# Optimization experiments

Measured on AMD Instinct MI355X. Metric: run time of the kernel, lower is better.

The kernel has to match this reference:

```python
import jax, jax.numpy as jnp
import numpy as np

BITS = 4
OFF = 8          # 2**(BITS-1)
QLEVELS = 15.0   # 2**BITS - 1
IN_F, OUT_F, FP_F, TOKENS = 4096, 4096, 256, 4096
INT_F = IN_F - FP_F


def unpack_i4(w_packed):
    """Invert pack_to_i4: packed uint8 col k holds signed int4 cols (2k: low nibble, 2k+1: high)."""
    lo = (w_packed & 0x0F).astype(jnp.int8)
    hi = ((w_packed >> 4) & 0x0F).astype(jnp.int8)
    lo = jnp.where(lo >= 8, lo - 16, lo)
    hi = jnp.where(hi >= 8, hi - 16, hi)
    return jnp.stack([lo, hi], axis=-1).reshape(w_packed.shape[0], -1)  # (out, int_features)


def setup_inputs() -> dict:
    key = jax.random.key(0)
    k1, k2, k3, k4, k5 = jax.random.split(key, 5)
    x = jax.random.normal(k1, (1, TOKENS, IN_F), dtype=jnp.float16)
    perm = jax.random.permutation(k2, IN_F)
    fp_indices = jnp.sort(perm[:FP_F]).astype(jnp.int64)
    int_indices = jnp.sort(perm[FP_F:]).astype(jnp.int64)
    # signed int4 weight values in [-8, 7], packed two-per-byte like pack_to_i4
    w_vals = jax.random.randint(k3, (OUT_F, INT_F), -8, 8, dtype=jnp.int8)
    u = (w_vals.astype(jnp.int32) & 0x0F).astype(jnp.uint8)
    int_weight = (u[:, 0::2] | (u[:, 1::2] << 4)).astype(jnp.uint8)  # (out, INT_F//2)
    weights_scales = (jax.random.uniform(k4, (OUT_F, 1)) * 0.01 + 1e-3).astype(jnp.float16)
    # reduced_w = row-sum of the dequantized int-column weights (as in from_float)
    reduced_w = (w_vals.astype(jnp.float32).sum(axis=1, keepdims=True)
                 * weights_scales.astype(jnp.float32)).T.astype(jnp.float16)  # (1, out)
    fp_weight = (jax.random.normal(k5, (OUT_F, FP_F)) * 0.02).astype(jnp.float16)
    bias = jnp.zeros((OUT_F,), dtype=jnp.float16)
    return {"x": x, "int_weight": int_weight, "weights_scales": weights_scales,
            "reduced_w": reduced_w, "fp_weight": fp_weight, "bias": bias,
            "int_indices": int_indices, "fp_indices": fp_indices}


def reference(x, int_weight, weights_scales, reduced_w, fp_weight, bias,
              int_indices, fp_indices):
    x2 = x[0]                                   # (M, in_features)
    int_x = x2[:, int_indices].astype(jnp.float32)   # (M, INT_F)
    fp_x = x2[:, fp_indices].astype(jnp.float32)     # (M, FP_F)
    # asymmetric per-row quantization to signed int4
    mn = int_x.min(axis=1, keepdims=True)
    mx = int_x.max(axis=1, keepdims=True)
    scale = jnp.maximum((mx - mn) / QLEVELS, 1e-8)   # (M,1)
    zero = mn                                        # (M,1)
    q = jnp.clip(jnp.round((int_x - zero) / scale) - OFF, -8, 7).astype(jnp.int8)
    w_int = unpack_i4(int_weight)                    # (out, INT_F) int8
    int_result = jnp.matmul(q.astype(jnp.int32), w_int.T.astype(jnp.int32))  # (M, out) int32
    fp_result = fp_x @ fp_weight.T.astype(jnp.float32) + bias.astype(jnp.float32)
    # asym dequant: x ~ (q + OFF)*scale + zero, W = w_int * w_scale, sum_j W_j = reduced_w
    w_scale = weights_scales.astype(jnp.float32)[:, 0][None, :]   # (1, out)
    out = (scale * w_scale * int_result.astype(jnp.float32)
           + (zero + scale * OFF) * reduced_w.astype(jnp.float32)
           + fp_result)
    return out.astype(jnp.float16)[None]             # (1, M, out)
```

## Files before the change

kernel.cpp:

```cpp
#include <hip/hip_runtime.h>
#include <hip/hip_bf16.h>

#define IN_FEAT 4096
#define OUT_FEAT 4096
#define FP_FEAT 256
#define INT_FEAT 3840
#define TOKENS 4096
#define PACKED_W (INT_FEAT / 2)

#define NT_I8 60
#define NT_ALL 68

typedef __attribute__((ext_vector_type(8))) short short8;
typedef __attribute__((ext_vector_type(4))) float f32x4;
typedef __attribute__((ext_vector_type(4))) int   int32x4;

#define AQ8_OFF   0u
#define WB8_OFF   16777216u
#define AFP_OFF   33554432u
#define WFP_OFF   35651584u
#define SCALE_OFF 37748736u
#define ZERO_OFF  37765120u
#define WS_NEED   37781504u

__global__ __launch_bounds__(256) void prep_kernel(
    const float* __restrict__ x,
    const int* __restrict__ int_idx_raw,
    const int* __restrict__ fp_idx_raw,
    const int* __restrict__ wpacked_raw,
    const float* __restrict__ fpw,
    const float* __restrict__ wscale,
    signed char* __restrict__ Aq8,
    __hip_bfloat16* __restrict__ Afp,
    signed char* __restrict__ Wb8,
    __hip_bfloat16* __restrict__ Wfp,
    float* __restrict__ scale_ws,
    float* __restrict__ zero_ws)
{
    const int t = threadIdx.x;
    if (blockIdx.x < TOKENS) {
        const int m = blockIdx.x;
        const float* xr = x + (size_t)m * IN_FEAT;
        const bool is64 = (int_idx_raw[1] == 0) && (int_idx_raw[3] == 0);

        float v[15];
        float mn = 1e30f, mx = -1e30f;
#pragma unroll
        for (int j = 0; j < 15; ++j) {
            int k = t + j * 256;
            int idx = is64 ? int_idx_raw[2 * k] : int_idx_raw[k];
            float f = xr[idx];
            v[j] = f;
            mn = fminf(mn, f);
            mx = fmaxf(mx, f);
        }
#pragma unroll
        for (int off = 1; off < 64; off <<= 1) {
            mn = fminf(mn, __shfl_xor(mn, off));
            mx = fmaxf(mx, __shfl_xor(mx, off));
        }
        __shared__ float smn[4], smx[4];
        int wid = t >> 6, lane = t & 63;
        if (lane == 0) { smn[wid] = mn; smx[wid] = mx; }
        __syncthreads();
        if (t == 0) {
            float rmn = fminf(fminf(smn[0], smn[1]), fminf(smn[2], smn[3]));
            float rmx = fmaxf(fmaxf(smx[0], smx[1]), fmaxf(smx[2], smx[3]));
            float sc = fmaxf((rmx - rmn) / 15.0f, 1e-8f);
            smn[0] = rmn;
            smx[0] = sc;
            scale_ws[m] = sc;
            zero_ws[m] = rmn;
        }
        __syncthreads();
        const float zero = smn[0];
        const float sc = smx[0];

        signed char* ar = Aq8 + (size_t)m * INT_FEAT;
#pragma unroll
        for (int j = 0; j < 15; ++j) {
            int k = t + j * 256;
            float q = rintf((v[j] - zero) / sc) - 8.0f;
            q = fminf(fmaxf(q, -8.0f), 7.0f);
            ar[k] = (signed char)(int)q;
        }
        int fpi = is64 ? fp_idx_raw[2 * t] : fp_idx_raw[t];
        Afp[(size_t)m * FP_FEAT + t] = __float2bfloat16(xr[fpi] / sc);
    } else {
        const int n = blockIdx.x - TOKENS;
        bool is_i32 = true;
#pragma unroll
        for (int j = 0; j < 8; ++j) {
            unsigned w = (unsigned)wpacked_raw[j];
            if (w > 0xFFu) is_i32 = false;
        }
        short* wo = (short*)(Wb8 + (size_t)n * INT_FEAT);
#pragma unroll
        for (int j = 0; j < 8; ++j) {
            int k = t + j * 256;
            if (k < PACKED_W) {
                int p = is_i32 ? wpacked_raw[(size_t)n * PACKED_W + k]
                               : ((const unsigned char*)wpacked_raw)[(size_t)n * PACKED_W + k];
                int lo = p & 15; if (lo >= 8) lo -= 16;
                int hi = (p >> 4) & 15; if (hi >= 8) hi -= 16;
                wo[k] = (short)(((unsigned char)lo) | ((unsigned short)(unsigned char)hi << 8));
            }
        }
        float wsn = wscale[n];
        Wfp[(size_t)n * FP_FEAT + t] = __float2bfloat16(fpw[(size_t)n * FP_FEAT + t] / wsn);
    }
}


__global__ __launch_bounds__(512, 2) void gemm256_i8(
    const signed char* __restrict__ Aq8,
    const __hip_bfloat16* __restrict__ Afp,
    const signed char* __restrict__ Wb8,
    const __hip_bfloat16* __restrict__ Wfp,
    const float* __restrict__ scale_ws,
    const float* __restrict__ zero_ws,
    const float* __restrict__ wscale,
    const float* __restrict__ reduced,
    const float* __restrict__ bias,
    float* __restrict__ out)
{
    __shared__ __align__(16) char lds[131072];

    const int t = threadIdx.x;
    const int lane = t & 63, wid = t >> 6;
    const int wr = wid >> 2;
    const int wc = wid & 3;
    const int r16 = lane & 15;
    const int kg = lane >> 4;

    const int bid = blockIdx.x;
    const int sb = (bid & 7) * 32 + (bid >> 3);
    const int tileM = (sb >> 4) * 256;
    const int tileN = (sb & 15) * 256;

    const int id0 = t, id1 = 512 + t;
    const int r0 = id0 >> 2, c0 = id0 & 3;
    const int r1 = id1 >> 2, c1 = id1 & 3;
    const int sw0 = ((c0 ^ ((r0 >> 1) & 3)) << 4);
    const int sw1 = ((c1 ^ ((r1 >> 1) & 3)) << 4);
    const char* a8_0 = (const char*)Aq8 + (size_t)(tileM + r0) * INT_FEAT + sw0;
    const char* a8_1 = (const char*)Aq8 + (size_t)(tileM + r1) * INT_FEAT + sw1;
    const char* b8_0 = (const char*)Wb8 + (size_t)(tileN + r0) * INT_FEAT + sw0;
    const char* b8_1 = (const char*)Wb8 + (size_t)(tileN + r1) * INT_FEAT + sw1;
    const char* af_0 = (const char*)Afp + (size_t)(tileM + r0) * 512 + sw0;
    const char* af_1 = (const char*)Afp + (size_t)(tileM + r1) * 512 + sw1;
    const char* bf_0 = (const char*)Wfp + (size_t)(tileN + r0) * 512 + sw0;
    const char* bf_1 = (const char*)Wfp + (size_t)(tileN + r1) * 512 + sw1;
    const int dst0 = id0 << 4, dst1 = id1 << 4;

    auto stage = [&](int vt, int bufB) {
        const char *pa0, *pa1, *pb0, *pb1;
        if (vt < NT_I8) {
            int ko = vt * 64;
            pa0 = a8_0 + ko; pa1 = a8_1 + ko; pb0 = b8_0 + ko; pb1 = b8_1 + ko;
        } else {
            int ko = (vt - NT_I8) * 64;
            pa0 = af_0 + ko; pa1 = af_1 + ko; pb0 = bf_0 + ko; pb1 = bf_1 + ko;
        }
        __builtin_amdgcn_global_load_lds(
            (const __attribute__((address_space(1))) void*)pa0,
            (__attribute__((address_space(3))) void*)(lds + bufB + dst0), 16, 0, 0);
        __builtin_amdgcn_global_load_lds(
            (const __attribute__((address_space(1))) void*)pa1,
            (__attribute__((address_space(3))) void*)(lds + bufB + dst1), 16, 0, 0);
        __builtin_amdgcn_global_load_lds(
            (const __attribute__((address_space(1))) void*)pb0,
            (__attribute__((address_space(3))) void*)(lds + bufB + 16384 + dst0), 16, 0, 0);
        __builtin_amdgcn_global_load_lds(
            (const __attribute__((address_space(1))) void*)pb1,
            (__attribute__((address_space(3))) void*)(lds + bufB + 16384 + dst1), 16, 0, 0);
    };

    int aOff[8], bOff[4];
#pragma unroll
    for (int mf = 0; mf < 8; ++mf) {
        int ra = wr * 128 + mf * 16 + r16;
        aOff[mf] = ra * 64 + ((((ra >> 1) & 3) ^ kg) << 4);
    }
#pragma unroll
    for (int nf = 0; nf < 4; ++nf) {
        int rb = wc * 64 + nf * 16 + r16;
        bOff[nf] = 16384 + rb * 64 + ((((rb >> 1) & 3) ^ kg) << 4);
    }

    int32x4 acc[8][4];
#pragma unroll
    for (int mf = 0; mf < 8; ++mf)
#pragma unroll
        for (int nf = 0; nf < 4; ++nf)
            acc[mf][nf] = (int32x4){0, 0, 0, 0};

    stage(0, 0);
    stage(1, 32768);
    stage(2, 65536);
    asm volatile("s_waitcnt vmcnt(8)" ::: "memory");
    __builtin_amdgcn_sched_barrier(0);
    __builtin_amdgcn_s_barrier();
    __builtin_amdgcn_sched_barrier(0);

    for (int vt = 0; vt < NT_I8; ++vt) {
        const int bufB = (vt & 3) << 15;
        int32x4 bI[4], aI[8];
#pragma unroll
        for (int nf = 0; nf < 4; ++nf)
            bI[nf] = *(const int32x4*)(lds + bufB + bOff[nf]);
#pragma unroll
        for (int mf = 0; mf < 8; ++mf)
            aI[mf] = *(const int32x4*)(lds + bufB + aOff[mf]);

        stage(vt + 3, ((vt + 3) & 3) << 15);

        __builtin_amdgcn_s_setprio(1);
#pragma unroll
        for (int mf = 0; mf < 8; ++mf)
#pragma unroll
            for (int nf = 0; nf < 4; ++nf)
                acc[mf][nf] = __builtin_amdgcn_mfma_i32_16x16x64_i8(
                    aI[mf], bI[nf], acc[mf][nf], 0, 0, 0);
        __builtin_amdgcn_s_setprio(0);

        asm volatile("s_waitcnt vmcnt(8)" ::: "memory");
        __builtin_amdgcn_sched_barrier(0);
        __builtin_amdgcn_s_barrier();
        __builtin_amdgcn_sched_barrier(0);
    }

#pragma unroll
    for (int mf = 0; mf < 8; ++mf)
#pragma unroll
        for (int nf = 0; nf < 4; ++nf) {
            int32x4 vi = acc[mf][nf];
            f32x4 vf;
#pragma unroll
            for (int i = 0; i < 4; ++i) vf[i] = (float)vi[i];
            acc[mf][nf] = __builtin_bit_cast(int32x4, vf);
        }

    for (int vt = NT_I8; vt < NT_ALL; ++vt) {
        const int bufB = (vt & 3) << 15;
        short8 bF[4], aF[8];
#pragma unroll
        for (int nf = 0; nf < 4; ++nf)
            bF[nf] = *(const short8*)(lds + bufB + bOff[nf]);
#pragma unroll
        for (int mf = 0; mf < 8; ++mf)
            aF[mf] = *(const short8*)(lds + bufB + aOff[mf]);

        if (vt + 3 < NT_ALL)
            stage(vt + 3, ((vt + 3) & 3) << 15);

        __builtin_amdgcn_s_setprio(1);
#pragma unroll
        for (int mf = 0; mf < 8; ++mf)
#pragma unroll
            for (int nf = 0; nf < 4; ++nf)
                acc[mf][nf] = __builtin_bit_cast(int32x4,
                    __builtin_amdgcn_mfma_f32_16x16x32_bf16(
                        aF[mf], bF[nf],
                        __builtin_bit_cast(f32x4, acc[mf][nf]), 0, 0, 0));
        __builtin_amdgcn_s_setprio(0);

        if (vt <= NT_ALL - 4)
            asm volatile("s_waitcnt vmcnt(8)" ::: "memory");
        else if (vt == NT_ALL - 3)
            asm volatile("s_waitcnt vmcnt(4)" ::: "memory");
        else if (vt == NT_ALL - 2)
            asm volatile("s_waitcnt vmcnt(0)" ::: "memory");
        __builtin_amdgcn_sched_barrier(0);
        __builtin_amdgcn_s_barrier();
        __builtin_amdgcn_sched_barrier(0);
    }

    const int cr4 = kg * 4;
#pragma unroll
    for (int mf = 0; mf < 8; ++mf) {
#pragma unroll
        for (int nf = 0; nf < 4; ++nf) {
            int n = tileN + wc * 64 + nf * 16 + r16;
            float ws = wscale[n];
            float rd = reduced[n];
            float bs = bias[n];
            f32x4 av = __builtin_bit_cast(f32x4, acc[mf][nf]);
#pragma unroll
            for (int i = 0; i < 4; ++i) {
                int m = tileM + wr * 128 + mf * 16 + cr4 + i;
                float sc = scale_ws[m];
                float zr = zero_ws[m];
                out[(size_t)m * OUT_FEAT + n] =
                    sc * ws * av[i]
                    + (zr + sc * 8.0f) * rd + bs;
            }
        }
    }
}

extern "C" void kernel_launch(void* const* d_in, const int* in_sizes, int n_in,
                              void* d_out, int out_size, void* d_ws, size_t ws_size,
                              hipStream_t stream)
{
    const void* px = 0; const void* pw = 0; const void* pfpw = 0;
    const void* pii = 0; const void* pfi = 0;
    const void* p4096[3] = {0, 0, 0}; int n4096 = 0;
    for (int i = 0; i < n_in; ++i) {
        switch (in_sizes[i]) {
            case 16777216: px = d_in[i]; break;
            case 7864320:  pw = d_in[i]; break;
            case 1048576:  pfpw = d_in[i]; break;
            case 3840:     pii = d_in[i]; break;
            case 256:      pfi = d_in[i]; break;
            case 4096:     if (n4096 < 3) p4096[n4096++] = d_in[i]; break;
            default: break;
        }
    }
    if (!px || !pw || !pfpw || !pii || !pfi || n4096 != 3) return;

    const float* x       = (const float*)px;
    const int*   wpacked = (const int*)pw;
    const float* wscale  = (const float*)p4096[0];
    const float* reduced = (const float*)p4096[1];
    const float* bias    = (const float*)p4096[2];
    const float* fpw     = (const float*)pfpw;
    const int*   int_idx = (const int*)pii;
    const int*   fp_idx  = (const int*)pfi;
    float*       out     = (float*)d_out;

    if (ws_size < (size_t)WS_NEED) return;

    char* ws = (char*)d_ws;
    signed char*    Aq8 = (signed char*)(ws + AQ8_OFF);
    signed char*    Wb8 = (signed char*)(ws + WB8_OFF);
    __hip_bfloat16* Afp = (__hip_bfloat16*)(ws + AFP_OFF);
    __hip_bfloat16* Wfp = (__hip_bfloat16*)(ws + WFP_OFF);
    float* scale_ws     = (float*)(ws + SCALE_OFF);
    float* zero_ws      = (float*)(ws + ZERO_OFF);

    prep_kernel<<<TOKENS + OUT_FEAT, 256, 0, stream>>>(
        x, int_idx, fp_idx, wpacked, fpw, wscale,
        Aq8, Afp, Wb8, Wfp, scale_ws, zero_ws);
    gemm256_i8<<<256, 512, 0, stream>>>(Aq8, Afp, Wb8, Wfp,
                                        scale_ws, zero_ws,
                                        wscale, reduced, bias, out);
}
```

Measured before the change: 98.71 us.

## Process two K-tiles per barrier with prefetch distance two

Restructures the main int8 and bf16 MFMA loops to handle two K-tiles between each workgroup barrier, halving the number of s_barrier/waitcnt synchronisation points. Prefetch distance drops from three tiles ahead to two, and each barrier now waits for all outstanding loads (vmcnt(0)) instead of leaving some in flight. This trades less barrier overhead for reduced load/compute overlap, since loads issued in the second half-step must fully land before the next pair starts. The stage lambda is also rewritten with selects instead of branches.

```diff
diff --git a/kernel.cpp b/kernel.cpp
--- a/kernel.cpp
+++ b/kernel.cpp
@@ -154,14 +154,12 @@
     const int dst0 = id0 << 4, dst1 = id1 << 4;
 
     auto stage = [&](int vt, int bufB) {
-        const char *pa0, *pa1, *pb0, *pb1;
-        if (vt < NT_I8) {
-            int ko = vt * 64;
-            pa0 = a8_0 + ko; pa1 = a8_1 + ko; pb0 = b8_0 + ko; pb1 = b8_1 + ko;
-        } else {
-            int ko = (vt - NT_I8) * 64;
-            pa0 = af_0 + ko; pa1 = af_1 + ko; pb0 = bf_0 + ko; pb1 = bf_1 + ko;
-        }
+        const bool i8p = vt < NT_I8;
+        const int ko = i8p ? vt * 64 : (vt - NT_I8) * 64;
+        const char* pa0 = (i8p ? a8_0 : af_0) + ko;
+        const char* pa1 = (i8p ? a8_1 : af_1) + ko;
+        const char* pb0 = (i8p ? b8_0 : bf_0) + ko;
+        const char* pb1 = (i8p ? b8_1 : bf_1) + ko;
         __builtin_amdgcn_global_load_lds(
             (const __attribute__((address_space(1))) void*)pa0,
             (__attribute__((address_space(3))) void*)(lds + bufB + dst0), 16, 0, 0);
@@ -197,38 +195,41 @@
 
     stage(0, 0);
     stage(1, 32768);
-    stage(2, 65536);
-    asm volatile("s_waitcnt vmcnt(8)" ::: "memory");
+    asm volatile("s_waitcnt vmcnt(0)" ::: "memory");
     __builtin_amdgcn_sched_barrier(0);
     __builtin_amdgcn_s_barrier();
     __builtin_amdgcn_sched_barrier(0);
 
-    for (int vt = 0; vt < NT_I8; ++vt) {
-        const int bufB = (vt & 3) << 15;
-        int32x4 bI[4], aI[8];
-#pragma unroll
-        for (int nf = 0; nf < 4; ++nf)
-            bI[nf] = *(const int32x4*)(lds + bufB + bOff[nf]);
-#pragma unroll
-        for (int mf = 0; mf < 8; ++mf)
-            aI[mf] = *(const int32x4*)(lds + bufB + aOff[mf]);
-
-        stage(vt + 3, ((vt + 3) & 3) << 15);
-
-        __builtin_amdgcn_s_setprio(1);
-#pragma unroll
-        for (int mf = 0; mf < 8; ++mf)
-#pragma unroll
-            for (int nf = 0; nf < 4; ++nf)
-                acc[mf][nf] = __builtin_amdgcn_mfma_i32_16x16x64_i8(
-                    aI[mf], bI[nf], acc[mf][nf], 0, 0, 0);
-        __builtin_amdgcn_s_setprio(0);
-
-        asm volatile("s_waitcnt vmcnt(8)" ::: "memory");
+#define TILE_I8_BODY(VT)                                                       \
+    {                                                                          \
+        const int bufB = ((VT) & 3) << 15;                                     \
+        int32x4 bI[4], aI[8];                                                  \
+        _Pragma("unroll")                                                      \
+        for (int nf = 0; nf < 4; ++nf)                                         \
+            bI[nf] = *(const int32x4*)(lds + bufB + bOff[nf]);                 \
+        _Pragma("unroll")                                                      \
+        for (int mf = 0; mf < 8; ++mf)                                         \
+            aI[mf] = *(const int32x4*)(lds + bufB + aOff[mf]);                 \
+        stage((VT) + 2, (((VT) + 2) & 3) << 15);                               \
+        __builtin_amdgcn_s_setprio(1);                                         \
+        _Pragma("unroll")                                                      \
+        for (int mf = 0; mf < 8; ++mf)                                         \
+            _Pragma("unroll")                                                  \
+            for (int nf = 0; nf < 4; ++nf)                                     \
+                acc[mf][nf] = __builtin_amdgcn_mfma_i32_16x16x64_i8(           \
+                    aI[mf], bI[nf], acc[mf][nf], 0, 0, 0);                     \
+        __builtin_amdgcn_s_setprio(0);                                         \
+    }
+
+    for (int vt = 0; vt < NT_I8; vt += 2) {
+        TILE_I8_BODY(vt);
+        TILE_I8_BODY(vt + 1);
+        asm volatile("s_waitcnt vmcnt(0)" ::: "memory");
         __builtin_amdgcn_sched_barrier(0);
         __builtin_amdgcn_s_barrier();
         __builtin_amdgcn_sched_barrier(0);
     }
+#undef TILE_I8_BODY
 
 #pragma unroll
     for (int mf = 0; mf < 8; ++mf)
@@ -241,40 +242,39 @@
             acc[mf][nf] = __builtin_bit_cast(int32x4, vf);
         }
 
-    for (int vt = NT_I8; vt < NT_ALL; ++vt) {
-        const int bufB = (vt & 3) << 15;
-        short8 bF[4], aF[8];
-#pragma unroll
-        for (int nf = 0; nf < 4; ++nf)
-            bF[nf] = *(const short8*)(lds + bufB + bOff[nf]);
-#pragma unroll
-        for (int mf = 0; mf < 8; ++mf)
-            aF[mf] = *(const short8*)(lds + bufB + aOff[mf]);
-
-        if (vt + 3 < NT_ALL)
-            stage(vt + 3, ((vt + 3) & 3) << 15);
-
-        __builtin_amdgcn_s_setprio(1);
-#pragma unroll
-        for (int mf = 0; mf < 8; ++mf)
-#pragma unroll
-            for (int nf = 0; nf < 4; ++nf)
-                acc[mf][nf] = __builtin_bit_cast(int32x4,
-                    __builtin_amdgcn_mfma_f32_16x16x32_bf16(
-                        aF[mf], bF[nf],
-                        __builtin_bit_cast(f32x4, acc[mf][nf]), 0, 0, 0));
-        __builtin_amdgcn_s_setprio(0);
-
-        if (vt <= NT_ALL - 4)
-            asm volatile("s_waitcnt vmcnt(8)" ::: "memory");
-        else if (vt == NT_ALL - 3)
-            asm volatile("s_waitcnt vmcnt(4)" ::: "memory");
-        else if (vt == NT_ALL - 2)
-            asm volatile("s_waitcnt vmcnt(0)" ::: "memory");
+#define TILE_FP_BODY(VT)                                                       \
+    {                                                                          \
+        const int bufB = ((VT) & 3) << 15;                                     \
+        short8 bF[4], aF[8];                                                   \
+        _Pragma("unroll")                                                      \
+        for (int nf = 0; nf < 4; ++nf)                                         \
+            bF[nf] = *(const short8*)(lds + bufB + bOff[nf]);                  \
+        _Pragma("unroll")                                                      \
+        for (int mf = 0; mf < 8; ++mf)                                         \
+            aF[mf] = *(const short8*)(lds + bufB + aOff[mf]);                  \
+        if ((VT) + 2 < NT_ALL)                                                 \
+            stage((VT) + 2, (((VT) + 2) & 3) << 15);                           \
+        __builtin_amdgcn_s_setprio(1);                                         \
+        _Pragma("unroll")                                                      \
+        for (int mf = 0; mf < 8; ++mf)                                         \
+            _Pragma("unroll")                                                  \
+            for (int nf = 0; nf < 4; ++nf)                                     \
+                acc[mf][nf] = __builtin_bit_cast(int32x4,                      \
+                    __builtin_amdgcn_mfma_f32_16x16x32_bf16(                   \
+                        aF[mf], bF[nf],                                        \
+                        __builtin_bit_cast(f32x4, acc[mf][nf]), 0, 0, 0));     \
+        __builtin_amdgcn_s_setprio(0);                                         \
+    }
+
+    for (int vt = NT_I8; vt < NT_ALL; vt += 2) {
+        TILE_FP_BODY(vt);
+        TILE_FP_BODY(vt + 1);
+        asm volatile("s_waitcnt vmcnt(0)" ::: "memory");
         __builtin_amdgcn_sched_barrier(0);
         __builtin_amdgcn_s_barrier();
         __builtin_amdgcn_sched_barrier(0);
     }
+#undef TILE_FP_BODY
 
     const int cr4 = kg * 4;
 #pragma unroll
```

After: 98.18 us. No clear change (-0.5%).
